# Kernel tuning notes

Measured on AMD Instinct MI355X. Metric: run time of the kernel, lower is better.

## Reference

```python
import jax, jax.numpy as jnp
import numpy as np

KERNEL_SIZE = 4  # W


def setup_inputs() -> dict:
    key = jax.random.key(0)
    k1, k2, k3, k4 = jax.random.split(key, 4)
    B, T, D, H, W = 2, 4096, 2048, 2048, KERNEL_SIZE
    x = jax.random.normal(k1, (B, T, D), dtype=jnp.float32)
    # torch nn.Linear weight layout: [out_features, in_features]
    w1 = jax.random.normal(k2, (H, D), dtype=jnp.float32) * 0.02
    w2_w = jax.random.normal(k3, (D * W, H), dtype=jnp.float32) * 0.02
    w2_b = jax.random.normal(k4, (D * W,), dtype=jnp.float32) * 0.02
    return {"x": x, "w1": w1, "w2_w": w2_w, "w2_b": w2_b}


def reference(x, w1, w2_w, w2_b):
    # x: [B, T, D]
    B, T, D = x.shape
    W = KERNEL_SIZE
    # kernel generator MLP: Linear(D->H, no bias) -> silu -> Linear(H->D*W, bias)
    h = jax.nn.silu(jnp.einsum('btd,hd->bth', x, w1))
    flat_kernels = jnp.einsum('bth,kh->btk', h, w2_w) + w2_b
    # rearrange 'b t (d w) -> b t d w' (d major, w minor)
    kernels = flat_kernels.reshape(B, T, D, W)
    # causal windows: pad W-1 on the left of time, gather W shifted views
    x_pad = jnp.pad(x, ((0, 0), (W - 1, 0), (0, 0)))
    windows = jnp.stack([x_pad[:, w:w + T, :] for w in range(W)], axis=-1)  # [B,T,D,W]
    out = jnp.sum(windows * kernels, axis=-1)  # per-token dynamic depthwise causal conv
    return jax.nn.silu(out)  # self.activation == 'silu'
```

## Files before the change

kernel.cpp:

```cpp
#include <hip/hip_runtime.h>
#include <hip/hip_bf16.h>
#include <math.h>

#define B_DIM 2
#define T_DIM 4096
#define D_DIM 2048
#define H_DIM 2048
#define W_K   4
#define M_DIM (B_DIM * T_DIM)
#define N2_DIM (D_DIM * W_K)

typedef __bf16 bf16x8 __attribute__((ext_vector_type(8)));
typedef float  f32x4  __attribute__((ext_vector_type(4)));

#define BM 256
#define BN 256
#define BKT 64
#define XW_STRIDE 68

__device__ __forceinline__ unsigned short f2bf(float f) {
    unsigned int u = __float_as_uint(f);
    unsigned int r = (u + 0x7FFFu + ((u >> 16) & 1u)) >> 16;
    return (unsigned short)r;
}

__device__ __forceinline__ float silu_f(float v) {
    return v / (1.0f + __expf(-v));
}

__global__ void cvt_f32_to_bf16(const float* __restrict__ in,
                                unsigned short* __restrict__ out, int n4) {
    int i = blockIdx.x * blockDim.x + threadIdx.x;
    if (i >= n4) return;
    float4 v = reinterpret_cast<const float4*>(in)[i];
    ushort4 o;
    o.x = f2bf(v.x); o.y = f2bf(v.y); o.z = f2bf(v.z); o.w = f2bf(v.w);
    reinterpret_cast<ushort4*>(out)[i] = o;
}

__device__ __forceinline__ bf16x8 lds_frag(const unsigned short* buf, int r, int kb) {
    int sx = (((r & 7) ^ ((r >> 3) & 7)) << 4);
    int lin = r * 128 + (kb ^ sx);
    return *reinterpret_cast<const bf16x8*>(reinterpret_cast<const char*>(buf) + lin);
}

#define BARRIER()    __builtin_amdgcn_s_barrier()
#define WAIT_VM(N)   asm volatile("s_waitcnt vmcnt(" #N ")" ::: "memory")

#define STAGE64(basePtr, ko, dstUshort, chunk) \
    __builtin_amdgcn_global_load_lds( \
        (const __attribute__((address_space(1))) void*)((basePtr) + soff + (size_t)(chunk) * 64 * K + (ko)), \
        (__attribute__((address_space(3))) void*)(reinterpret_cast<char*>(dstUshort) + ((chunk) << 13) + (wave << 10)), \
        16, 0, 0)

#define MG_MFMA(mg, AF) \
    _Pragma("unroll") for (int kk = 0; kk < 2; ++kk) \
    _Pragma("unroll") for (int mrel = 0; mrel < 2; ++mrel) \
    _Pragma("unroll") for (int nf = 0; nf < 4; ++nf) \
        acc[(mg)*2 + mrel][nf] = __builtin_amdgcn_mfma_f32_16x16x32_bf16( \
            AF[mrel][kk], bfrag[nf][kk], acc[(mg)*2 + mrel][nf], 0, 0, 0)

#define READ_B(tB) \
    _Pragma("unroll") for (int nf = 0; nf < 4; ++nf) \
    _Pragma("unroll") for (int kk = 0; kk < 2; ++kk) \
        bfrag[nf][kk] = lds_frag(tB, wc*64 + ln15*4 + nf, kk*64 + kb16)

#define READ_A(AF, tA, mg) \
    _Pragma("unroll") for (int mrel = 0; mrel < 2; ++mrel) \
    _Pragma("unroll") for (int kk = 0; kk < 2; ++kk) \
        AF[mrel][kk] = lds_frag(tA, wr*128 + (mg)*32 + mrel*16 + ln15, kk*64 + kb16)

#define KTILE_R(bi, jj, SA2, SB, VMN) do { \
    const unsigned short* tA = smem + (bi) * 16384; \
    const unsigned short* tB = smem + 32768 + (bi) * 16384; \
    unsigned short* oA = smem + ((bi) ^ 1) * 16384; \
    unsigned short* cA = smem + (bi) * 16384; \
    unsigned short* cB = smem + 32768 + (bi) * 16384; \
    READ_B(tB); \
    READ_A(af0, tA, 0); \
    if (SA2) { const int ko = ((jj) + 1) << 6; \
        STAGE64(baseA, ko, oA, 1); STAGE64(baseA, ko, oA, 3); } \
    READ_A(af1, tA, 1); \
    __builtin_amdgcn_s_setprio(1); MG_MFMA(0, af0); __builtin_amdgcn_s_setprio(0); \
    __builtin_amdgcn_s_setprio(1); MG_MFMA(1, af1); __builtin_amdgcn_s_setprio(0); \
    BARRIER(); \
    READ_A(af0, tA, 2); \
    if (SB) { const int ko = ((jj) + 2) << 6; \
        STAGE64(baseB, ko, cB, 0); STAGE64(baseB, ko, cB, 1); \
        STAGE64(baseA, ko, cA, 0); STAGE64(baseA, ko, cA, 2); } \
    READ_A(af1, tA, 3); \
    __builtin_amdgcn_s_setprio(1); MG_MFMA(2, af0); __builtin_amdgcn_s_setprio(0); \
    if (SB) { const int ko = ((jj) + 2) << 6; \
        STAGE64(baseB, ko, cB, 2); STAGE64(baseB, ko, cB, 3); } \
    __builtin_amdgcn_s_setprio(1); MG_MFMA(3, af1); __builtin_amdgcn_s_setprio(0); \
    WAIT_VM(VMN); \
    BARRIER(); \
} while (0)

template <int EPI>
__global__ __launch_bounds__(512, 2)
void gemm8p(const unsigned short* __restrict__ A,
            const unsigned short* __restrict__ Bm,
            int M, int N, int K,
            unsigned short* __restrict__ Hout,
            const float* __restrict__ bias,
            const float* __restrict__ Xf,
            float* __restrict__ Out) {
    __shared__ __align__(16) unsigned short smem[65536];

    const int tid  = threadIdx.x;
    const int wave = tid >> 6, lane = tid & 63;
    const int wr = wave >> 2, wc = wave & 3;
    const int ln15 = lane & 15;
    const int kb16 = (lane >> 4) * 16;

    const int GX = gridDim.x, GY = gridDim.y;
    const int bid = blockIdx.y * GX + blockIdx.x;
    const int xcd = bid & 7;
    const int idx = bid >> 3;
    const int W_ = GX >> 2;
    const int rr = idx / W_, cc = idx % W_;
    const int by = (xcd >> 2) * (GY >> 1) + rr;
    const int bx = (xcd & 3) * W_ + cc;
    const int m0 = by * BM, n0 = bx * BN;

    const int nk = K >> 6;

    const int srow = (wave << 3) + (lane >> 3);
    const int scol = (((lane & 7) ^ (lane >> 3) ^ wave) << 3);
    const size_t soff = (size_t)srow * K + scol;
    const unsigned short* baseA = A + (size_t)m0 * K;
    const unsigned short* baseB = Bm + (size_t)n0 * K;

    f32x4 acc[8][4];
#pragma unroll
    for (int i = 0; i < 8; ++i)
#pragma unroll
        for (int j = 0; j < 4; ++j) acc[i][j] = (f32x4)0.0f;

    bf16x8 bfrag[4][2], af0[2][2], af1[2][2];

    {
        unsigned short* dA0 = smem;
        unsigned short* dB0 = smem + 32768;
        unsigned short* dA1 = smem + 16384;
        unsigned short* dB1 = smem + 49152;
        STAGE64(baseB, 0, dB0, 0); STAGE64(baseB, 0, dB0, 1);
        STAGE64(baseB, 0, dB0, 2); STAGE64(baseB, 0, dB0, 3);
        STAGE64(baseA, 0, dA0, 0); STAGE64(baseA, 0, dA0, 1);
        STAGE64(baseA, 0, dA0, 2); STAGE64(baseA, 0, dA0, 3);
        STAGE64(baseB, BKT, dB1, 0); STAGE64(baseB, BKT, dB1, 1);
        STAGE64(baseA, BKT, dA1, 0); STAGE64(baseA, BKT, dA1, 2);
        STAGE64(baseB, BKT, dB1, 2); STAGE64(baseB, BKT, dB1, 3);
    }
    WAIT_VM(6);
    BARRIER();

    for (int it = 0; it < (nk >> 1) - 1; ++it) {
        const int j = it << 1;
        KTILE_R(0, j,     1, 1, 6);
        KTILE_R(1, j + 1, 1, 1, 6);
    }
    KTILE_R(0, nk - 2, 1, 0, 0);
    KTILE_R(1, nk - 1, 0, 0, 0);

    if (EPI == 0) {
        const size_t colbase = n0 + wc * 64 + ln15 * 4;
#pragma unroll
        for (int mf = 0; mf < 8; ++mf) {
            int rowb = m0 + wr * 128 + mf * 16 + (lane >> 4) * 4;
#pragma unroll
            for (int r2 = 0; r2 < 4; ++r2) {
                ushort4 h4;
                h4.x = f2bf(silu_f(acc[mf][0][r2]));
                h4.y = f2bf(silu_f(acc[mf][1][r2]));
                h4.z = f2bf(silu_f(acc[mf][2][r2]));
                h4.w = f2bf(silu_f(acc[mf][3][r2]));
                *reinterpret_cast<ushort4*>(&Hout[(size_t)(rowb + r2) * N + colbase]) = h4;
            }
        }
    } else {
        const int t0 = m0 & (T_DIM - 1);
        const int bidx = m0 >> 12;
        const int dbase = n0 >> 2;
        float* Xw = reinterpret_cast<float*>(smem);
        for (int idx2 = tid; idx2 < 259 * 16; idx2 += 512) {
            int rw = idx2 >> 4, q = (idx2 & 15) << 2;
            int ts = t0 - 3 + rw;
            float4 v = make_float4(0.f, 0.f, 0.f, 0.f);
            if (ts >= 0)
                v = *reinterpret_cast<const float4*>(
                    &Xf[((size_t)bidx * T_DIM + ts) * D_DIM + dbase + q]);
            float* p = &Xw[rw * XW_STRIDE + q];
            p[0] = v.x; p[1] = v.y; p[2] = v.z; p[3] = v.w;
        }
        __syncthreads();

        const int dloc = wc * 16 + ln15;
        const float4 bias4 = *reinterpret_cast<const float4*>(
            &bias[n0 + wc * 64 + ln15 * 4]);
#pragma unroll
        for (int mf = 0; mf < 8; ++mf) {
            int lrow0 = wr * 128 + mf * 16 + (lane >> 4) * 4;
            float xr[7];
#pragma unroll
            for (int q = 0; q < 7; ++q)
                xr[q] = Xw[(lrow0 + q) * XW_STRIDE + dloc];
#pragma unroll
            for (int r2 = 0; r2 < 4; ++r2) {
                float v = (acc[mf][0][r2] + bias4.x) * xr[r2 + 0];
                v      += (acc[mf][1][r2] + bias4.y) * xr[r2 + 1];
                v      += (acc[mf][2][r2] + bias4.z) * xr[r2 + 2];
                v      += (acc[mf][3][r2] + bias4.w) * xr[r2 + 3];
                int lrow = lrow0 + r2;
                Out[((size_t)bidx * T_DIM + (t0 + lrow)) * D_DIM + dbase + dloc] = silu_f(v);
            }
        }
    }
}

extern "C" void kernel_launch(void* const* d_in, const int* in_sizes, int n_in,
                              void* d_out, int out_size, void* d_ws, size_t ws_size,
                              hipStream_t stream) {
    const float* x    = (const float*)d_in[0];
    const float* w1   = (const float*)d_in[1];
    const float* w2w  = (const float*)d_in[2];
    const float* w2b  = (const float*)d_in[3];
    float* out = (float*)d_out;

    unsigned short* ws0 = (unsigned short*)d_ws;
    unsigned short* ws1 = ws0 + (size_t)M_DIM * D_DIM;
    unsigned short* ws2 = ws1 + (size_t)H_DIM * D_DIM;

    const int CT = 256;
    {
        int n4 = (M_DIM * D_DIM) / 4;
        cvt_f32_to_bf16<<<(n4 + CT - 1) / CT, CT, 0, stream>>>(x, ws0, n4);
    }
    {
        int n4 = (H_DIM * D_DIM) / 4;
        cvt_f32_to_bf16<<<(n4 + CT - 1) / CT, CT, 0, stream>>>(w1, ws1, n4);
    }
    gemm8p<0><<<dim3(H_DIM / BN, M_DIM / BM), 512, 0, stream>>>(
        ws0, ws1, M_DIM, H_DIM, D_DIM, ws2, nullptr, nullptr, nullptr);
    {
        int n4 = (N2_DIM * H_DIM) / 4;
        cvt_f32_to_bf16<<<(n4 + CT - 1) / CT, CT, 0, stream>>>(w2w, ws0, n4);
    }
    gemm8p<1><<<dim3(N2_DIM / BN, M_DIM / BM), 512, 0, stream>>>(
        ws2, ws0, M_DIM, N2_DIM, H_DIM, nullptr, w2b, x, out);
}
```

Before: 369.5 us.

## Switch GEMM mainloop to BK=32 with three-stage LDS ring buffer

```diff
diff --git a/kernel.cpp b/kernel.cpp
--- a/kernel.cpp
+++ b/kernel.cpp
@@ -15,7 +15,7 @@
 
 #define BM 256
 #define BN 256
-#define BKT 64
+#define BKT 32
 #define XW_STRIDE 68
 
 __device__ __forceinline__ unsigned short f2bf(float f) {
@@ -39,60 +39,49 @@
 }
 
 __device__ __forceinline__ bf16x8 lds_frag(const unsigned short* buf, int r, int kb) {
-    int sx = (((r & 7) ^ ((r >> 3) & 7)) << 4);
-    int lin = r * 128 + (kb ^ sx);
+    int s = ((r >> 7) << 2) | (kb >> 4);
+    int p = s ^ (r & 7);
+    int lin = (r & 127) * 128 + (p << 4);
     return *reinterpret_cast<const bf16x8*>(reinterpret_cast<const char*>(buf) + lin);
 }
 
 #define BARRIER()    __builtin_amdgcn_s_barrier()
 #define WAIT_VM(N)   asm volatile("s_waitcnt vmcnt(" #N ")" ::: "memory")
 
-#define STAGE64(basePtr, ko, dstUshort, chunk) \
+#define STAGE32(basePtr, soffX, ko, dstUshort, c) \
     __builtin_amdgcn_global_load_lds( \
-        (const __attribute__((address_space(1))) void*)((basePtr) + soff + (size_t)(chunk) * 64 * K + (ko)), \
-        (__attribute__((address_space(3))) void*)(reinterpret_cast<char*>(dstUshort) + ((chunk) << 13) + (wave << 10)), \
+        (const __attribute__((address_space(1))) void*)((basePtr) + (soffX) + (size_t)(c) * 64 * K + (ko)), \
+        (__attribute__((address_space(3))) void*)(reinterpret_cast<char*>(dstUshort) + ((c) << 13) + (wave << 10)), \
         16, 0, 0)
 
-#define MG_MFMA(mg, AF) \
-    _Pragma("unroll") for (int kk = 0; kk < 2; ++kk) \
-    _Pragma("unroll") for (int mrel = 0; mrel < 2; ++mrel) \
+#define READ_B4(tB) \
     _Pragma("unroll") for (int nf = 0; nf < 4; ++nf) \
-        acc[(mg)*2 + mrel][nf] = __builtin_amdgcn_mfma_f32_16x16x32_bf16( \
-            AF[mrel][kk], bfrag[nf][kk], acc[(mg)*2 + mrel][nf], 0, 0, 0)
-
-#define READ_B(tB) \
+        bfrag[nf] = lds_frag(tB, wc*64 + nf*16 + ln15, kb16)
+
+#define READ_A4(AF, tA, b) \
+    _Pragma("unroll") for (int i = 0; i < 4; ++i) \
+        AF[i] = lds_frag(tA, wr*128 + ((b)*4 + i)*16 + ln15, kb16)
+
+#define MG16(b, AF) \
+    _Pragma("unroll") for (int mi = 0; mi < 4; ++mi) \
     _Pragma("unroll") for (int nf = 0; nf < 4; ++nf) \
-    _Pragma("unroll") for (int kk = 0; kk < 2; ++kk) \
-        bfrag[nf][kk] = lds_frag(tB, wc*64 + ln15*4 + nf, kk*64 + kb16)
-
-#define READ_A(AF, tA, mg) \
-    _Pragma("unroll") for (int mrel = 0; mrel < 2; ++mrel) \
-    _Pragma("unroll") for (int kk = 0; kk < 2; ++kk) \
-        AF[mrel][kk] = lds_frag(tA, wr*128 + (mg)*32 + mrel*16 + ln15, kk*64 + kb16)
-
-#define KTILE_R(bi, jj, SA2, SB, VMN) do { \
-    const unsigned short* tA = smem + (bi) * 16384; \
-    const unsigned short* tB = smem + 32768 + (bi) * 16384; \
-    unsigned short* oA = smem + ((bi) ^ 1) * 16384; \
-    unsigned short* cA = smem + (bi) * 16384; \
-    unsigned short* cB = smem + 32768 + (bi) * 16384; \
-    READ_B(tB); \
-    READ_A(af0, tA, 0); \
-    if (SA2) { const int ko = ((jj) + 1) << 6; \
-        STAGE64(baseA, ko, oA, 1); STAGE64(baseA, ko, oA, 3); } \
-    READ_A(af1, tA, 1); \
-    __builtin_amdgcn_s_setprio(1); MG_MFMA(0, af0); __builtin_amdgcn_s_setprio(0); \
-    __builtin_amdgcn_s_setprio(1); MG_MFMA(1, af1); __builtin_amdgcn_s_setprio(0); \
-    BARRIER(); \
-    READ_A(af0, tA, 2); \
-    if (SB) { const int ko = ((jj) + 2) << 6; \
-        STAGE64(baseB, ko, cB, 0); STAGE64(baseB, ko, cB, 1); \
-        STAGE64(baseA, ko, cA, 0); STAGE64(baseA, ko, cA, 2); } \
-    READ_A(af1, tA, 3); \
-    __builtin_amdgcn_s_setprio(1); MG_MFMA(2, af0); __builtin_amdgcn_s_setprio(0); \
-    if (SB) { const int ko = ((jj) + 2) << 6; \
-        STAGE64(baseB, ko, cB, 2); STAGE64(baseB, ko, cB, 3); } \
-    __builtin_amdgcn_s_setprio(1); MG_MFMA(3, af1); __builtin_amdgcn_s_setprio(0); \
+        acc[(b)*4 + mi][nf] = __builtin_amdgcn_mfma_f32_16x16x32_bf16( \
+            AF[mi], bfrag[nf], acc[(b)*4 + mi][nf], 0, 0, 0)
+
+#define KTILE3(sR, sW, jj, SG, VMN) do { \
+    const unsigned short* tA = smem + (sR) * 8192; \
+    const unsigned short* tB = smem + 24576 + (sR) * 8192; \
+    unsigned short* dA = smem + (sW) * 8192; \
+    unsigned short* dB = smem + 24576 + (sW) * 8192; \
+    READ_B4(tB); \
+    if (SG) { const int ko = ((jj) + 2) << 5; \
+        STAGE32(baseB, soffB, ko, dB, 0); STAGE32(baseB, soffB, ko, dB, 1); } \
+    READ_A4(af0, tA, 0); \
+    if (SG) { const int ko = ((jj) + 2) << 5; \
+        STAGE32(baseA, soffA, ko, dA, 0); STAGE32(baseA, soffA, ko, dA, 1); } \
+    READ_A4(af1, tA, 1); \
+    __builtin_amdgcn_s_setprio(1); MG16(0, af0); __builtin_amdgcn_s_setprio(0); \
+    __builtin_amdgcn_s_setprio(1); MG16(1, af1); __builtin_amdgcn_s_setprio(0); \
     WAIT_VM(VMN); \
     BARRIER(); \
 } while (0)
@@ -106,7 +95,7 @@
             const float* __restrict__ bias,
             const float* __restrict__ Xf,
             float* __restrict__ Out) {
-    __shared__ __align__(16) unsigned short smem[65536];
+    __shared__ __align__(16) unsigned short smem[49152];
 
     const int tid  = threadIdx.x;
     const int wave = tid >> 6, lane = tid & 63;
@@ -124,11 +113,16 @@
     const int bx = (xcd & 3) * W_ + cc;
     const int m0 = by * BM, n0 = bx * BN;
 
-    const int nk = K >> 6;
-
-    const int srow = (wave << 3) + (lane >> 3);
-    const int scol = (((lane & 7) ^ (lane >> 3) ^ wave) << 3);
-    const size_t soff = (size_t)srow * K + scol;
+    const int nk = K >> 5;
+
+    const int frl  = (wave << 3) + (lane >> 3);
+    const int sl   = (lane & 7) ^ (lane >> 3);
+    const int kbu  = (sl & 3) << 3;
+    const int gA0  = frl + 128 * (sl >> 2);
+    const size_t soffA = (size_t)gA0 * K + kbu;
+    const int rho  = gA0 & 63;
+    const int prho = ((rho & 15) << 2) | (rho >> 4);
+    const size_t soffB = (size_t)(((gA0 >> 6) << 6) + prho) * K + kbu;
     const unsigned short* baseA = A + (size_t)m0 * K;
     const unsigned short* baseB = Bm + (size_t)n0 * K;
 
@@ -138,31 +132,29 @@
 #pragma unroll
         for (int j = 0; j < 4; ++j) acc[i][j] = (f32x4)0.0f;
 
-    bf16x8 bfrag[4][2], af0[2][2], af1[2][2];
-
-    {
-        unsigned short* dA0 = smem;
-        unsigned short* dB0 = smem + 32768;
-        unsigned short* dA1 = smem + 16384;
-        unsigned short* dB1 = smem + 49152;
-        STAGE64(baseB, 0, dB0, 0); STAGE64(baseB, 0, dB0, 1);
-        STAGE64(baseB, 0, dB0, 2); STAGE64(baseB, 0, dB0, 3);
-        STAGE64(baseA, 0, dA0, 0); STAGE64(baseA, 0, dA0, 1);
-        STAGE64(baseA, 0, dA0, 2); STAGE64(baseA, 0, dA0, 3);
-        STAGE64(baseB, BKT, dB1, 0); STAGE64(baseB, BKT, dB1, 1);
-        STAGE64(baseA, BKT, dA1, 0); STAGE64(baseA, BKT, dA1, 2);
-        STAGE64(baseB, BKT, dB1, 2); STAGE64(baseB, BKT, dB1, 3);
-    }
-    WAIT_VM(6);
+    bf16x8 bfrag[4], af0[4], af1[4];
+
+    {
+        unsigned short* a0 = smem;               unsigned short* b0 = smem + 24576;
+        unsigned short* a1 = smem + 8192;        unsigned short* b1 = smem + 32768;
+        STAGE32(baseB, soffB, 0, b0, 0);  STAGE32(baseB, soffB, 0, b0, 1);
+        STAGE32(baseA, soffA, 0, a0, 0);  STAGE32(baseA, soffA, 0, a0, 1);
+        STAGE32(baseB, soffB, 32, b1, 0); STAGE32(baseB, soffB, 32, b1, 1);
+        STAGE32(baseA, soffA, 32, a1, 0); STAGE32(baseA, soffA, 32, a1, 1);
+    }
+    WAIT_VM(4);
     BARRIER();
 
-    for (int it = 0; it < (nk >> 1) - 1; ++it) {
-        const int j = it << 1;
-        KTILE_R(0, j,     1, 1, 6);
-        KTILE_R(1, j + 1, 1, 1, 6);
-    }
-    KTILE_R(0, nk - 2, 1, 0, 0);
-    KTILE_R(1, nk - 1, 0, 0, 0);
+    for (int it = 0; it < (nk - 4) / 3; ++it) {
+        const int j = it * 3;
+        KTILE3(0, 2, j,     1, 4);
+        KTILE3(1, 0, j + 1, 1, 4);
+        KTILE3(2, 1, j + 2, 1, 4);
+    }
+    KTILE3(0, 2, nk - 4, 1, 4);
+    KTILE3(1, 0, nk - 3, 1, 4);
+    KTILE3(2, 1, nk - 2, 0, 0);
+    KTILE3(0, 2, nk - 1, 0, 0);
 
     if (EPI == 0) {
         const size_t colbase = n0 + wc * 64 + ln15 * 4;
```

Measured after the change: 351.1 us. -5.0%, faster.
